# Kernel tuning notes

Measured on AMD Instinct MI355X. Metric: run time of the kernel, lower is better.

## Reference

```python
import jax, jax.numpy as jnp
import numpy as np

EPS = 0.01
H, W = 300, 400
WORLD_SCALE = 400.0


def setup_inputs() -> dict:
    key = jax.random.key(0)
    ks = jax.random.split(key, 8)
    N, B, D, HID = 200000, 2, 256, 256
    fx = fy = 300.0
    cx, cy = W / 2.0, H / 2.0
    z = jax.random.uniform(ks[0], (N,), minval=2.0, maxval=10.0)
    u = jax.random.uniform(ks[1], (N,), minval=0.0, maxval=float(W))
    v = jax.random.uniform(ks[2], (N,), minval=0.0, maxval=float(H))
    vert_pos = jnp.stack([(u - cx) / fx * z, (v - cy) / fy * z, z], axis=0)  # [3,N]
    target_pose = jnp.tile(jnp.eye(4, dtype=jnp.float32)[None], (B, 1, 1))
    K = jnp.array([[fx, 0.0, cx], [0.0, fy, cy], [0.0, 0.0, 1.0]], dtype=jnp.float32)
    target_intrinsics = jnp.tile(K[None], (B, 1, 1))
    vert_feat = 0.1 * jax.random.normal(ks[3], (N, D), dtype=jnp.float32)
    vert_opy = jnp.ones((N,), dtype=jnp.float32)
    W1 = 0.05 * jax.random.normal(ks[4], (D + 3, HID), dtype=jnp.float32)
    b1 = jnp.zeros((HID,), dtype=jnp.float32)
    W2 = 0.05 * jax.random.normal(ks[5], (HID, 3), dtype=jnp.float32)
    b2 = jnp.zeros((3,), dtype=jnp.float32)
    bkg_col = jnp.zeros((3,), dtype=jnp.float32)
    ref_images = jax.random.normal(ks[6], (B, 3, H, W), dtype=jnp.float32)
    return {"vert_pos": vert_pos, "ref_images": ref_images, "target_pose": target_pose,
            "target_intrinsics": target_intrinsics, "vert_feat": vert_feat, "vert_opy": vert_opy,
            "W1": W1, "b1": b1, "W2": W2, "b2": b2, "bkg_col": bkg_col}


def reference(vert_pos, ref_images, target_pose, target_intrinsics,
              vert_feat, vert_opy, W1, b1, W2, b2, bkg_col):
    B = target_pose.shape[0]
    N = vert_pos.shape[1]
    # homogeneous world points, transform to target camera frame
    xyzw = jnp.concatenate([vert_pos, jnp.ones((1, N), vert_pos.dtype)], axis=0)  # [4,N]
    xyz_t = jnp.einsum('bij,jn->bin', target_pose, xyzw)[:, :3]                   # [B,3,N]
    xy_proj = jnp.einsum('bij,bjn->bin', target_intrinsics, xyz_t)                # [B,3,N]
    z = xy_proj[:, 2:3]
    eps_mask = jax.lax.stop_gradient(jnp.abs(z) < EPS)                            # [B,1,N]
    zs = jnp.where(eps_mask, EPS, z)
    uv = xy_proj[:, 0:2] / zs
    sampler = jnp.where(eps_mask, -1e6, jnp.concatenate([uv, zs], axis=1))        # [B,3,N]
    # view direction in world frame per point
    vnorm = xyz_t / jnp.linalg.norm(xyz_t, axis=1, keepdims=True)
    vh = jnp.concatenate([vnorm, jnp.zeros_like(vnorm[:, 0:1])], axis=1)          # [B,4,N]
    pose_inv = jnp.linalg.inv(target_pose)
    vdir = jnp.einsum('bij,bjn->bin', pose_inv, vh)[:, :3]                        # [B,3,N]
    vdir = vdir.transpose(0, 2, 1).reshape(B * N, 3)
    # per-point neural shading (MLP shader on concat(feat, view_dir))
    feat = jnp.broadcast_to(vert_feat[None], (B, N, vert_feat.shape[1])).reshape(B * N, -1)
    x = jnp.concatenate([feat, vdir], axis=-1)
    h = jax.nn.relu(x @ W1 + b1)
    rgb = jax.nn.sigmoid(h @ W2 + b2).reshape(B, N, 3)                            # [B,N,3]
    opacity = jnp.clip(jax.nn.sigmoid(vert_opy), 0.0, 1.0)                        # [N]
    # differentiable splat: scatter shaded colors weighted by opacity to pixels
    u_pix, v_pix, zz = sampler[:, 0], sampler[:, 1], sampler[:, 2]                # [B,N]
    ix = jnp.round(u_pix).astype(jnp.int32)
    iy = jnp.round(v_pix).astype(jnp.int32)
    valid = (ix >= 0) & (ix < W) & (iy >= 0) & (iy < H) & (zz >= 1.0)
    idx = jnp.where(valid, iy * W + ix, H * W)                                    # dump bin H*W
    wts = opacity[None, :] * valid.astype(rgb.dtype)                              # [B,N]
    seg = lambda vals, ids: jax.ops.segment_sum(vals, ids, num_segments=H * W + 1)
    num = jax.vmap(seg)(wts[..., None] * rgb, idx)[:, :H * W]                     # [B,HW,3]
    den = jax.vmap(seg)(wts, idx)[:, :H * W]                                      # [B,HW]
    fg = num / (den[..., None] + 1e-8)
    alpha = 1.0 - jnp.exp(-den)
    img = fg * alpha[..., None] + bkg_col * (1.0 - alpha[..., None])
    return img.reshape(B, H, W, 3).transpose(0, 3, 1, 2)                          # [B,3,H,W]
```

## Files before the change

### kernel.cpp

```cpp
#include <hip/hip_runtime.h>
#include <cstdint>
#include <cstddef>

#define HH 300
#define WW 400
#define HWPIX (HH*WW)

typedef __attribute__((ext_vector_type(8))) short short8_t;
typedef __attribute__((ext_vector_type(4))) float f32x4;

static __device__ __forceinline__ unsigned short f2bf(float f){
  union { float f; unsigned u; } v; v.f = f;
  unsigned r = (v.u + 0x7fffu + ((v.u >> 16) & 1u)) >> 16;
  return (unsigned short)r;
}
static __device__ __forceinline__ float bf2f(unsigned short us){
  union { unsigned u; float f; } v; v.u = ((unsigned)us) << 16;
  return v.f;
}
static __device__ __forceinline__ float dot4_x(float a0,float x0,float a1,float x1,
                                               float a2,float x2,float a3,float x3){
  #pragma clang fp contract(off)
  float s = a0*x0;
  s = s + a1*x1;
  s = s + a2*x2;
  s = s + a3*x3;
  return s;
}
static __device__ __forceinline__ float dot3_x(float a0,float x0,float a1,float x1,
                                               float a2,float x2){
  #pragma clang fp contract(off)
  float s = a0*x0;
  s = s + a1*x1;
  s = s + a2*x2;
  return s;
}

static __device__ __forceinline__ void gload_lds16(const void* g, void* l){
  __builtin_amdgcn_global_load_lds(
      (const __attribute__((address_space(1))) unsigned int*)g,
      (__attribute__((address_space(3))) unsigned int*)l, 16, 0, 0);
}

__global__ void prep_kernel(const float* __restrict__ W1, const float* __restrict__ W2,
                            const float* __restrict__ pose,
                            float* __restrict__ poseinv, unsigned short* __restrict__ W1aT,
                            float* __restrict__ ntab, int B){
  int tid = threadIdx.x;
  int bid = blockIdx.x;
  if (bid < 256){
    int k = bid, n = tid;
    int kt = k >> 6;
    int c8 = (k >> 3) & 7;
    int i  = k & 7;
    W1aT[kt*16384 + n*64 + ((c8 ^ (n & 7))*8) + i] = f2bf(W1[k*256 + n]);
  } else {
    int n = tid;
    ntab[n*8+0] = W1[256*256 + n];
    ntab[n*8+1] = W1[257*256 + n];
    ntab[n*8+2] = W1[258*256 + n];
    ntab[n*8+3] = W2[n*3+0];
    ntab[n*8+4] = W2[n*3+1];
    ntab[n*8+5] = W2[n*3+2];
    ntab[n*8+6] = 0.f; ntab[n*8+7] = 0.f;
    if (tid < B){
      float M[4][8];
      const float* A = pose + tid*16;
      for (int i=0;i<4;i++) for (int j=0;j<4;j++){ M[i][j]=A[i*4+j]; M[i][4+j] = (i==j)?1.f:0.f; }
      for (int c=0;c<4;c++){
        int p=c;
        for (int r=c+1;r<4;r++) if (fabsf(M[r][c])>fabsf(M[p][c])) p=r;
        if (p!=c) for (int j=0;j<8;j++){ float t=M[c][j]; M[c][j]=M[p][j]; M[p][j]=t; }
        float inv = 1.f/M[c][c];
        for (int j=0;j<8;j++) M[c][j]*=inv;
        for (int r=0;r<4;r++) if (r!=c){ float f=M[r][c]; for(int j=0;j<8;j++) M[r][j]-=f*M[c][j]; }
      }
      float* O = poseinv + tid*16;
      for (int i=0;i<4;i++) for (int j=0;j<4;j++) O[i*4+j]=M[i][4+j];
    }
  }
}

__global__ __launch_bounds__(256) void mlp_scatter_kernel(
    const float* __restrict__ feat, const unsigned short* __restrict__ W1aT,
    const float* __restrict__ b1, const float* __restrict__ b2,
    const float* __restrict__ ntab,
    const float* __restrict__ vp, const float* __restrict__ opy,
    const float* __restrict__ pose, const float* __restrict__ intr,
    const float* __restrict__ poseinv,
    float* __restrict__ num, float* __restrict__ den, int N, int B)
{
  __shared__ __align__(16) char smem[40960];
  unsigned short* sA = (unsigned short*)smem;
  unsigned short* sB = (unsigned short*)(smem + 8192);
  unsigned short* sH = (unsigned short*)smem;
  float* part        = (float*)(smem + 32768);

  const int tid  = threadIdx.x;
  const int lane = tid & 63;
  const int wv   = __builtin_amdgcn_readfirstlane(tid >> 6);
  const int lr   = lane & 15;
  const int qd   = lane >> 4;
  const int m0   = blockIdx.x * 64;

  f32x4 acc[4][4];
  for (int i=0;i<4;i++) for (int j=0;j<4;j++) acc[i][j] = (f32x4){0.f,0.f,0.f,0.f};

  ushort4 uA[4];
  {
    #pragma unroll
    for (int i=0;i<4;i++){
      int q   = i*256 + tid;
      int row = q >> 4;
      int c4  = q & 15;
      long rg = m0 + row; if (rg >= N) rg = N-1;
      float4 f = *(const float4*)(feat + rg*256 + c4*4);
      ushort4 u; u.x = f2bf(f.x); u.y = f2bf(f.y); u.z = f2bf(f.z); u.w = f2bf(f.w);
      uA[i] = u;
    }
  }

  for (int kt=0; kt<4; kt++){
    #pragma unroll
    for (int i=0;i<4;i++){
      int q   = i*256 + tid;
      int row = q >> 4;
      int c4  = q & 15;
      int q8 = c4 >> 1, half = c4 & 1;
      int phys = q8 ^ (row & 7);
      *(ushort4*)(sA + row*64 + phys*8 + half*4) = uA[i];
    }
    {
      const unsigned int* gim = (const unsigned int*)(W1aT + kt*16384);
      unsigned int* lim = (unsigned int*)sB;
      #pragma unroll
      for (int i=0;i<8;i++)
        gload_lds16(gim + i*1024 + tid*4, lim + i*1024 + tid*4);
    }
    __syncthreads();

    if (kt < 3){
      #pragma unroll
      for (int i=0;i<4;i++){
        int q   = i*256 + tid;
        int row = q >> 4;
        int c4  = q & 15;
        long rg = m0 + row; if (rg >= N) rg = N-1;
        float4 f = *(const float4*)(feat + rg*256 + (kt+1)*64 + c4*4);
        ushort4 u; u.x = f2bf(f.x); u.y = f2bf(f.y); u.z = f2bf(f.z); u.w = f2bf(f.w);
        uA[i] = u;
      }
    }

    #pragma unroll
    for (int ks=0; ks<2; ks++){
      short8_t av[4], bv[4];
      int qlog = ks*4 + qd;
      #pragma unroll
      for (int mt=0; mt<4; mt++){
        int row  = mt*16 + lr;
        int phys = qlog ^ (row & 7);
        av[mt] = *(const short8_t*)(sA + row*64 + phys*8);
      }
      #pragma unroll
      for (int nt=0; nt<4; nt++){
        int n    = wv*64 + nt*16 + lr;
        int phys = qlog ^ (n & 7);
        bv[nt] = *(const short8_t*)(sB + n*64 + phys*8);
      }
      #pragma unroll
      for (int mt=0; mt<4; mt++)
        #pragma unroll
        for (int nt=0; nt<4; nt++)
          acc[mt][nt] = __builtin_amdgcn_mfma_f32_16x16x32_bf16(av[mt], bv[nt], acc[mt][nt], 0,0,0);
    }
    __syncthreads();
  }

  #pragma unroll
  for (int nt=0; nt<4; nt++){
    int n = wv*64 + nt*16 + lr;
    float bias = b1[n];
    int c = n >> 3, e = n & 7;
    #pragma unroll
    for (int mt=0; mt<4; mt++)
      #pragma unroll
      for (int rr=0; rr<4; rr++){
        int m = mt*16 + qd*4 + rr;
        sH[m*256 + ((c ^ (m & 7))<<3) + e] = f2bf(acc[mt][nt][rr] + bias);
      }
  }
  __syncthreads();

  const int r = lane;
  long vg = m0 + r;
  bool rowok = vg < N; if (!rowok) vg = N-1;
  float px = vp[vg], py = vp[(size_t)N+vg], pz = vp[2*(size_t)N+vg];
  const float* tb = ntab + (size_t)wv*64*8;
  const int rsw = r & 7;
  const unsigned short* hrow = sH + r*256;
  float opac = 1.f/(1.f+expf(-opy[vg]));

  for (int b0=0; b0<B; b0+=2){
    int nb = (B - b0 < 2) ? (B - b0) : 2;
    float s_up=-1e6f, s_vp=-1e6f, s_zz=-1e6f;
    for (int bi=0; bi<nb; bi++){
      int b = b0 + bi;
      const float* P  = pose + b*16;
      const float* Kc = intr + b*9;
      const float* Pi = poseinv + b*16;
      float xt = dot4_x(P[0],px, P[1],py, P[2], pz, P[3], 1.f);
      float yt = dot4_x(P[4],px, P[5],py, P[6], pz, P[7], 1.f);
      float zt = dot4_x(P[8],px, P[9],py, P[10],pz, P[11],1.f);
      float uu = dot3_x(Kc[0],xt, Kc[1],yt, Kc[2],zt);
      float vv = dot3_x(Kc[3],xt, Kc[4],yt, Kc[5],zt);
      float zp = dot3_x(Kc[6],xt, Kc[7],yt, Kc[8],zt);
      bool em = fabsf(zp) < 0.01f;
      float zsafe = em ? 0.01f : zp;
      float up   = em ? -1e6f : uu/zsafe;
      float vpix = em ? -1e6f : vv/zsafe;
      float zz   = em ? -1e6f : zsafe;
      if (bi == wv){ s_up = up; s_vp = vpix; s_zz = zz; }
      float inrm = 1.f/sqrtf(xt*xt + yt*yt + zt*zt);
      float nx=xt*inrm, ny=yt*inrm, nz=zt*inrm;
      float vdx = Pi[0]*nx + Pi[1]*ny + Pi[2]*nz;
      float vdy = Pi[4]*nx + Pi[5]*ny + Pi[6]*nz;
      float vdz = Pi[8]*nx + Pi[9]*ny + Pi[10]*nz;

      float a0=0.f, a1=0.f, a2=0.f;
      #pragma unroll
      for (int j8=0;j8<8;j8++){
        int c = wv*8 + j8;
        short8_t hv = *(const short8_t*)(hrow + ((c ^ rsw)<<3));
        const float* t = tb + j8*64;
        #pragma unroll
        for (int e=0;e<8;e++){
          float h = bf2f((unsigned short)hv[e]) + vdx*t[e*8+0] + vdy*t[e*8+1] + vdz*t[e*8+2];
          h = fmaxf(h, 0.f);
          a0 += h*t[e*8+3]; a1 += h*t[e*8+4]; a2 += h*t[e*8+5];
        }
      }
      part[bi*768 + (wv*64 + r)*3 + 0] = a0;
      part[bi*768 + (wv*64 + r)*3 + 1] = a1;
      part[bi*768 + (wv*64 + r)*3 + 2] = a2;
    }
    __syncthreads();
    if (wv < nb){
      int b = b0 + wv;
      const float* pp = part + wv*768;
      float s0 = pp[r*3+0] + pp[(64+r)*3+0] + pp[(128+r)*3+0] + pp[(192+r)*3+0];
      float s1 = pp[r*3+1] + pp[(64+r)*3+1] + pp[(128+r)*3+1] + pp[(192+r)*3+1];
      float s2 = pp[r*3+2] + pp[(64+r)*3+2] + pp[(128+r)*3+2] + pp[(192+r)*3+2];
      float r0 = 1.f/(1.f+expf(-(s0 + b2[0])));
      float r1 = 1.f/(1.f+expf(-(s1 + b2[1])));
      float r2 = 1.f/(1.f+expf(-(s2 + b2[2])));
      int ix = (int)rintf(s_up);
      int iy = (int)rintf(s_vp);
      bool valid = rowok && ix>=0 && ix<WW && iy>=0 && iy<HH && s_zz>=1.0f;
      if (valid){
        int idx = iy*WW + ix;
        atomicAdd(den + (size_t)b*HWPIX + idx, opac);
        atomicAdd(num + ((size_t)b*3+0)*HWPIX + idx, opac*r0);
        atomicAdd(num + ((size_t)b*3+1)*HWPIX + idx, opac*r1);
        atomicAdd(num + ((size_t)b*3+2)*HWPIX + idx, opac*r2);
      }
    }
    __syncthreads();
  }
}

__global__ void compose_kernel(float* __restrict__ out, const float* __restrict__ den,
                               const float* __restrict__ bkg, int B){
  int i = blockIdx.x*256 + threadIdx.x;
  int total = B*HWPIX;
  if (i >= total) return;
  int b = i / HWPIX;
  int pix = i - b*HWPIX;
  float d = den[i];
  float alpha = 1.f - expf(-d);
  float om = 1.f - alpha;
  float dd = d + 1e-8f;
  float* ob = out + (size_t)b*3*HWPIX;
  float f0 = ob[0*HWPIX + pix] / dd;
  float f1 = ob[1*HWPIX + pix] / dd;
  float f2 = ob[2*HWPIX + pix] / dd;
  ob[0*HWPIX + pix] = f0*alpha + bkg[0]*om;
  ob[1*HWPIX + pix] = f1*alpha + bkg[1]*om;
  ob[2*HWPIX + pix] = f2*alpha + bkg[2]*om;
}

extern "C" void kernel_launch(void* const* d_in, const int* in_sizes, int n_in,
                              void* d_out, int out_size, void* d_ws, size_t ws_size,
                              hipStream_t stream){
  const float* vp   = (const float*)d_in[0];
  const float* pose = (const float*)d_in[2];
  const float* intr = (const float*)d_in[3];
  const float* feat = (const float*)d_in[4];
  const float* opy  = (const float*)d_in[5];
  const float* W1   = (const float*)d_in[6];
  const float* b1   = (const float*)d_in[7];
  const float* W2   = (const float*)d_in[8];
  const float* b2   = (const float*)d_in[9];
  const float* bkg  = (const float*)d_in[10];
  float* out = (float*)d_out;
  int N = in_sizes[0]/3;
  int B = in_sizes[2]/16;

  char* ws = (char*)d_ws;
  float* poseinv        = (float*)ws;
  unsigned short* W1aT  = (unsigned short*)(ws + 256);
  float* ntab           = (float*)(ws + 256 + 131072);
  float* den            = (float*)(ws + 256 + 131072 + 8192);

  hipMemsetAsync(out, 0, (size_t)out_size*sizeof(float), stream);
  hipMemsetAsync(den, 0, (size_t)B*HWPIX*sizeof(float), stream);
  prep_kernel<<<257, 256, 0, stream>>>(W1, W2, pose, poseinv, W1aT, ntab, B);
  int gridM = (N + 63)/64;
  mlp_scatter_kernel<<<gridM, 256, 0, stream>>>(feat, W1aT, b1, b2, ntab, vp, opy,
                                                pose, intr, poseinv, out, den, N, B);
  compose_kernel<<<(B*HWPIX + 255)/256, 256, 0, stream>>>(out, den, bkg, B);
}
```

Baseline: 437.0 us.

## Pack splat accumulators per pixel and spread atomics across all four waves

Splat accumulators move from separate planar num/den buffers into one interleaved float4-per-pixel buffer, so the four atomics for a point land in a single cache line. The atomic work is split so waves 0-1 handle red plus density and waves 2-3 handle green and blue. W1 tiles are now prefetched into registers and stored to LDS instead of using direct global-to-LDS loads, and the trailing barrier is skipped when no further batch follows. The compose pass reads one float4 per pixel, and the separate zeroing of the output is dropped. The cost is more register pressure from the uB prefetch and a larger workspace buffer to clear.

```diff
diff --git a/kernel.cpp b/kernel.cpp
--- a/kernel.cpp
+++ b/kernel.cpp
@@ -34,12 +34,6 @@
   s = s + a1*x1;
   s = s + a2*x2;
   return s;
-}
-
-static __device__ __forceinline__ void gload_lds16(const void* g, void* l){
-  __builtin_amdgcn_global_load_lds(
-      (const __attribute__((address_space(1))) unsigned int*)g,
-      (__attribute__((address_space(3))) unsigned int*)l, 16, 0, 0);
 }
 
 __global__ void prep_kernel(const float* __restrict__ W1, const float* __restrict__ W2,
@@ -88,7 +82,7 @@
     const float* __restrict__ vp, const float* __restrict__ opy,
     const float* __restrict__ pose, const float* __restrict__ intr,
     const float* __restrict__ poseinv,
-    float* __restrict__ num, float* __restrict__ den, int N, int B)
+    float* __restrict__ packed, int N, int B)
 {
   __shared__ __align__(16) char smem[40960];
   unsigned short* sA = (unsigned short*)smem;
@@ -107,6 +101,7 @@
   for (int i=0;i<4;i++) for (int j=0;j<4;j++) acc[i][j] = (f32x4){0.f,0.f,0.f,0.f};
 
   ushort4 uA[4];
+  uint4   uB[8];
   {
     #pragma unroll
     for (int i=0;i<4;i++){
@@ -118,6 +113,9 @@
       ushort4 u; u.x = f2bf(f.x); u.y = f2bf(f.y); u.z = f2bf(f.z); u.w = f2bf(f.w);
       uA[i] = u;
     }
+    const uint4* gim = (const uint4*)W1aT;
+    #pragma unroll
+    for (int i=0;i<8;i++) uB[i] = gim[i*256 + tid];
   }
 
   for (int kt=0; kt<4; kt++){
@@ -130,13 +128,9 @@
       int phys = q8 ^ (row & 7);
       *(ushort4*)(sA + row*64 + phys*8 + half*4) = uA[i];
     }
-    {
-      const unsigned int* gim = (const unsigned int*)(W1aT + kt*16384);
-      unsigned int* lim = (unsigned int*)sB;
-      #pragma unroll
-      for (int i=0;i<8;i++)
-        gload_lds16(gim + i*1024 + tid*4, lim + i*1024 + tid*4);
-    }
+    #pragma unroll
+    for (int i=0;i<8;i++)
+      ((uint4*)sB)[i*256 + tid] = uB[i];
     __syncthreads();
 
     if (kt < 3){
@@ -150,6 +144,9 @@
         ushort4 u; u.x = f2bf(f.x); u.y = f2bf(f.y); u.z = f2bf(f.z); u.w = f2bf(f.w);
         uA[i] = u;
       }
+      const uint4* gim = (const uint4*)W1aT + (size_t)(kt+1)*2048;
+      #pragma unroll
+      for (int i=0;i<8;i++) uB[i] = gim[i*256 + tid];
     }
 
     #pragma unroll
@@ -220,7 +217,7 @@
       float up   = em ? -1e6f : uu/zsafe;
       float vpix = em ? -1e6f : vv/zsafe;
       float zz   = em ? -1e6f : zsafe;
-      if (bi == wv){ s_up = up; s_vp = vpix; s_zz = zz; }
+      if (bi == (wv & 1)){ s_up = up; s_vp = vpix; s_zz = zz; }
       float inrm = 1.f/sqrtf(xt*xt + yt*yt + zt*zt);
       float nx=xt*inrm, ny=yt*inrm, nz=zt*inrm;
       float vdx = Pi[0]*nx + Pi[1]*ny + Pi[2]*nz;
@@ -245,48 +242,49 @@
       part[bi*768 + (wv*64 + r)*3 + 2] = a2;
     }
     __syncthreads();
-    if (wv < nb){
-      int b = b0 + wv;
-      const float* pp = part + wv*768;
-      float s0 = pp[r*3+0] + pp[(64+r)*3+0] + pp[(128+r)*3+0] + pp[(192+r)*3+0];
-      float s1 = pp[r*3+1] + pp[(64+r)*3+1] + pp[(128+r)*3+1] + pp[(192+r)*3+1];
-      float s2 = pp[r*3+2] + pp[(64+r)*3+2] + pp[(128+r)*3+2] + pp[(192+r)*3+2];
-      float r0 = 1.f/(1.f+expf(-(s0 + b2[0])));
-      float r1 = 1.f/(1.f+expf(-(s1 + b2[1])));
-      float r2 = 1.f/(1.f+expf(-(s2 + b2[2])));
+    if ((wv & 1) < nb){
+      int b = b0 + (wv & 1);
+      const float* pp = part + (wv & 1)*768;
       int ix = (int)rintf(s_up);
       int iy = (int)rintf(s_vp);
       bool valid = rowok && ix>=0 && ix<WW && iy>=0 && iy<HH && s_zz>=1.0f;
       if (valid){
-        int idx = iy*WW + ix;
-        atomicAdd(den + (size_t)b*HWPIX + idx, opac);
-        atomicAdd(num + ((size_t)b*3+0)*HWPIX + idx, opac*r0);
-        atomicAdd(num + ((size_t)b*3+1)*HWPIX + idx, opac*r1);
-        atomicAdd(num + ((size_t)b*3+2)*HWPIX + idx, opac*r2);
-      }
-    }
-    __syncthreads();
-  }
-}
-
-__global__ void compose_kernel(float* __restrict__ out, const float* __restrict__ den,
+        float* pkp = packed + ((size_t)b*HWPIX + (size_t)(iy*WW + ix))*4;
+        if (wv < 2){
+          float s0 = pp[r*3+0] + pp[(64+r)*3+0] + pp[(128+r)*3+0] + pp[(192+r)*3+0];
+          float r0 = 1.f/(1.f+expf(-(s0 + b2[0])));
+          atomicAdd(pkp + 3, opac);
+          atomicAdd(pkp + 0, opac*r0);
+        } else {
+          float s1 = pp[r*3+1] + pp[(64+r)*3+1] + pp[(128+r)*3+1] + pp[(192+r)*3+1];
+          float s2 = pp[r*3+2] + pp[(64+r)*3+2] + pp[(128+r)*3+2] + pp[(192+r)*3+2];
+          float r1 = 1.f/(1.f+expf(-(s1 + b2[1])));
+          float r2 = 1.f/(1.f+expf(-(s2 + b2[2])));
+          atomicAdd(pkp + 1, opac*r1);
+          atomicAdd(pkp + 2, opac*r2);
+        }
+      }
+    }
+    if (b0 + 2 < B) __syncthreads();
+  }
+}
+
+__global__ void compose_kernel(float* __restrict__ out, const float* __restrict__ pk,
                                const float* __restrict__ bkg, int B){
   int i = blockIdx.x*256 + threadIdx.x;
   int total = B*HWPIX;
   if (i >= total) return;
   int b = i / HWPIX;
   int pix = i - b*HWPIX;
-  float d = den[i];
+  float4 v = ((const float4*)pk)[i];
+  float d = v.w;
   float alpha = 1.f - expf(-d);
   float om = 1.f - alpha;
   float dd = d + 1e-8f;
   float* ob = out + (size_t)b*3*HWPIX;
-  float f0 = ob[0*HWPIX + pix] / dd;
-  float f1 = ob[1*HWPIX + pix] / dd;
-  float f2 = ob[2*HWPIX + pix] / dd;
-  ob[0*HWPIX + pix] = f0*alpha + bkg[0]*om;
-  ob[1*HWPIX + pix] = f1*alpha + bkg[1]*om;
-  ob[2*HWPIX + pix] = f2*alpha + bkg[2]*om;
+  ob[0*HWPIX + pix] = (v.x/dd)*alpha + bkg[0]*om;
+  ob[1*HWPIX + pix] = (v.y/dd)*alpha + bkg[1]*om;
+  ob[2*HWPIX + pix] = (v.z/dd)*alpha + bkg[2]*om;
 }
 
 extern "C" void kernel_launch(void* const* d_in, const int* in_sizes, int n_in,
@@ -310,13 +308,12 @@
   float* poseinv        = (float*)ws;
   unsigned short* W1aT  = (unsigned short*)(ws + 256);
   float* ntab           = (float*)(ws + 256 + 131072);
-  float* den            = (float*)(ws + 256 + 131072 + 8192);
-
-  hipMemsetAsync(out, 0, (size_t)out_size*sizeof(float), stream);
-  hipMemsetAsync(den, 0, (size_t)B*HWPIX*sizeof(float), stream);
+  float* packed         = (float*)(ws + 256 + 131072 + 8192);
+
+  hipMemsetAsync(packed, 0, (size_t)B*HWPIX*4*sizeof(float), stream);
   prep_kernel<<<257, 256, 0, stream>>>(W1, W2, pose, poseinv, W1aT, ntab, B);
   int gridM = (N + 63)/64;
   mlp_scatter_kernel<<<gridM, 256, 0, stream>>>(feat, W1aT, b1, b2, ntab, vp, opy,
-                                                pose, intr, poseinv, out, den, N, B);
-  compose_kernel<<<(B*HWPIX + 255)/256, 256, 0, stream>>>(out, den, bkg, B);
-}
+                                                pose, intr, poseinv, packed, N, B);
+  compose_kernel<<<(B*HWPIX + 255)/256, 256, 0, stream>>>(out, packed, bkg, B);
+}
```

Result: slower. 603.9 us (+38.2%).
